# Kernel tuning notes

Measured on AMD Instinct MI355X. Metric: run time of the kernel, lower is better.

Reference implementation:

```python
import math
import jax, jax.numpy as jnp
import numpy as np

B, T, C, H, DQK, DV = 2, 2048, 1024, 16, 64, 64


def setup_inputs() -> dict:
    key = jax.random.key(0)
    ks = jax.random.split(key, 5)
    x = jax.random.normal(ks[0], (B, T, C), dtype=jnp.float32)
    # randw: randn(*d) / sqrt(d[-1])
    w_q = jax.random.normal(ks[1], (H, DQK, C), dtype=jnp.float32) / math.sqrt(C)
    w_k = jax.random.normal(ks[2], (H, DQK, C), dtype=jnp.float32) / math.sqrt(C)
    w_v = jax.random.normal(ks[3], (H, DV, C), dtype=jnp.float32) / math.sqrt(C)
    w_o = jax.random.normal(ks[4], (DV * H, C), dtype=jnp.float32) / math.sqrt(C)
    return {"x": x, "w_q": w_q, "w_k": w_k, "w_v": w_v, "w_o": w_o}


def reference(x, w_q, w_k, w_v, w_o):
    # Full-sequence causal forward (bs_q.first == 0, nb == T): caches are
    # fully written in one shot, so they reduce to the plain projections.
    n, t, c = x.shape
    q = jnp.einsum('ntc,hdc->nhtd', x, w_q)
    k = jnp.einsum('ntc,hdc->nhtd', x, w_k)
    v = jnp.einsum('ntc,hdc->nhtd', x, w_v)
    scale = 1.0 / math.sqrt(w_q.shape[1])
    a = jnp.einsum('nhtd,nhsd->nhts', q, k) * scale  # [n,h,t,s]
    causal = jnp.arange(t)[:, None] < jnp.arange(t)[None, :]  # True above diag
    a = jnp.where(causal[None, None, :, :], -jnp.inf, a)
    a = jax.nn.softmax(a, axis=3)
    y = jnp.einsum('nhts,nhsd->nthd', a, v).reshape(n, t, -1)  # [n,t,h*dv]
    return y @ w_o  # cache_y, [n,t,c]
```

## Files before the change

### kernel.cpp

```cpp
#include <hip/hip_runtime.h>


typedef short bf16x8 __attribute__((ext_vector_type(8)));
typedef float f32x4 __attribute__((ext_vector_type(4)));

#define MFMA_BF16 __builtin_amdgcn_mfma_f32_16x16x32_bf16

#define QSCALE 0.18033688011112042f

__device__ __forceinline__ unsigned short f2bf(float f) {
    union { float f; unsigned u; } un; un.f = f;
    unsigned r = un.u + 0x7fffu + ((un.u >> 16) & 1u);
    return (unsigned short)(r >> 16);
}
__device__ __forceinline__ unsigned short f2bf_trunc(float f) {
    union { float f; unsigned u; } un; un.f = f;
    return (unsigned short)(un.u >> 16);
}
__device__ __forceinline__ unsigned pk2(float a, float b) {
    return (unsigned)f2bf(a) | ((unsigned)f2bf(b) << 16);
}
__device__ __forceinline__ void gload16(const void* g, void* l) {
    __builtin_amdgcn_global_load_lds(
        (const __attribute__((address_space(1))) unsigned int*)g,
        (__attribute__((address_space(3))) unsigned int*)l, 16, 0, 0);
}

__global__ __launch_bounds__(256) void prep(
    const float* __restrict__ x, const float* __restrict__ wq,
    const float* __restrict__ wk, const float* __restrict__ wv,
    const float* __restrict__ wo,
    unsigned short* __restrict__ x16, unsigned short* __restrict__ wq16,
    unsigned short* __restrict__ wk16, unsigned short* __restrict__ wv16,
    unsigned short* __restrict__ wot)
{
    const int bid = blockIdx.x;
    if (bid < 3584) {
        const float* s; unsigned short* d; int off;
        if (bid < 2048)      { s = x;  d = x16;  off = bid * 2048; }
        else if (bid < 2560) { s = wq; d = wq16; off = (bid - 2048) * 2048; }
        else if (bid < 3072) { s = wk; d = wk16; off = (bid - 2560) * 2048; }
        else                 { s = wv; d = wv16; off = (bid - 3072) * 2048; }
        int i = off + threadIdx.x * 8;
        float4 f0 = *(const float4*)&s[i], f1 = *(const float4*)&s[i + 4];
        uint4 o;
        o.x = pk2(f0.x, f0.y); o.y = pk2(f0.z, f0.w);
        o.z = pk2(f1.x, f1.y); o.w = pk2(f1.z, f1.w);
        *(uint4*)&d[i] = o;
    } else {
        __shared__ unsigned short t[64 * 72];
        const int b2 = bid - 3584;
        const int k0 = (b2 & 15) << 6, n0 = (b2 >> 4) << 6;
        const int r = threadIdx.x >> 2, cg = (threadIdx.x & 3) << 4;
        const float* src = &wo[(k0 + r) * 1024 + n0 + cg];
        #pragma unroll
        for (int j = 0; j < 16; j += 4) {
            float4 f = *(const float4*)&src[j];
            t[(cg + j + 0) * 72 + r] = f2bf(f.x);
            t[(cg + j + 1) * 72 + r] = f2bf(f.y);
            t[(cg + j + 2) * 72 + r] = f2bf(f.z);
            t[(cg + j + 3) * 72 + r] = f2bf(f.w);
        }
        __syncthreads();
        unsigned short* dst = &wot[(n0 + r) * 1024 + k0 + cg];
        unsigned short* tr = &t[r * 72 + cg];
        unsigned v[16];
        #pragma unroll
        for (int j = 0; j < 16; ++j) v[j] = tr[j];
        uint4 o0, o1;
        o0.x = v[0] | (v[1] << 16);   o0.y = v[2] | (v[3] << 16);
        o0.z = v[4] | (v[5] << 16);   o0.w = v[6] | (v[7] << 16);
        o1.x = v[8] | (v[9] << 16);   o1.y = v[10] | (v[11] << 16);
        o1.z = v[12] | (v[13] << 16); o1.w = v[14] | (v[15] << 16);
        *(uint4*)&dst[0] = o0;
        *(uint4*)&dst[8] = o1;
    }
}

__device__ __forceinline__ void gemm_body(
    const unsigned short* __restrict__ A, const unsigned short* __restrict__ Bm,
    void* __restrict__ C, int m0, int n0, int mode, int ldc, float sc)
{
    __shared__ unsigned short sa[128 * 64];
    __shared__ unsigned short sb[128 * 64];
    const int tid = threadIdx.x, wave = tid >> 6, lane = tid & 63;
    const int l15 = lane & 15, l4 = lane >> 4;
    const int wm = (wave >> 1) << 6, wn = (wave & 1) << 6;
    const int lrow = lane >> 3, lcb = (lane & 7) << 3;

    f32x4 acc[4][4] = {};

    for (int k0 = 0; k0 < 1024; k0 += 64) {
        #pragma unroll
        for (int i = 0; i < 4; ++i) {
            int rbase = i * 32 + wave * 8;
            gload16(&A[(size_t)(m0 + rbase + lrow) * 1024 + k0 + lcb], &sa[rbase * 64]);
            gload16(&Bm[(size_t)(n0 + rbase + lrow) * 1024 + k0 + lcb], &sb[rbase * 64]);
        }
        __syncthreads();
        #pragma unroll
        for (int ks = 0; ks < 2; ++ks) {
            bf16x8 af[4], bf[4];
            #pragma unroll
            for (int i = 0; i < 4; ++i)
                af[i] = *(const bf16x8*)&sa[(wm + i * 16 + l15) * 64 + ks * 32 + l4 * 8];
            #pragma unroll
            for (int j = 0; j < 4; ++j)
                bf[j] = *(const bf16x8*)&sb[(wn + j * 16 + l15) * 64 + ks * 32 + l4 * 8];
            #pragma unroll
            for (int i = 0; i < 4; ++i)
                #pragma unroll
                for (int j = 0; j < 4; ++j)
                    acc[i][j] = MFMA_BF16(af[i], bf[j], acc[i][j], 0, 0, 0);
        }
        __syncthreads();
    }

    #pragma unroll
    for (int i = 0; i < 4; ++i)
        #pragma unroll
        for (int j = 0; j < 4; ++j)
            #pragma unroll
            for (int r = 0; r < 4; ++r) {
                int row = m0 + wm + i * 16 + l4 * 4 + r;
                int col = n0 + wn + j * 16 + l15;
                float val = acc[i][j][r];
                if (mode == 0) {
                    int nb = row >> 11, t = row & 2047;
                    int hh = col >> 6, dd = col & 63;
                    ((unsigned short*)C)[(((nb << 4) + hh) * 2048 + t) * 64 + dd] =
                        f2bf(val * sc);
                } else if (mode == 1) {
                    ((float*)C)[(size_t)row * ldc + col] = val;
                } else {
                    ((unsigned short*)C)[(size_t)row * ldc + col] = f2bf(val);
                }
            }
}

__global__ __launch_bounds__(256) void proj(
    const unsigned short* __restrict__ x16,
    const unsigned short* __restrict__ wq16,
    const unsigned short* __restrict__ wk16,
    const unsigned short* __restrict__ wv16,
    unsigned short* __restrict__ qbuf,
    unsigned short* __restrict__ kbuf,
    unsigned short* __restrict__ vtb)
{
    const int bid = blockIdx.x;
    if (bid < 512) {
        int m0 = (bid & 31) << 7;
        int n0g = (bid >> 5) << 7;
        if (n0g < 1024)
            gemm_body(x16, wq16, qbuf, m0, n0g, 0, 0, QSCALE);
        else
            gemm_body(x16, wk16, kbuf, m0, n0g - 1024, 0, 0, 1.0f);
    } else {
        int v = bid - 512;
        gemm_body(wv16, x16, vtb, (v & 7) << 7, (v >> 3) << 7, 2, 4096, 1.0f);
    }
}

__global__ __launch_bounds__(256) void outp(
    const unsigned short* __restrict__ ybuf,
    const unsigned short* __restrict__ wot,
    float* __restrict__ out)
{
    const int bid = blockIdx.x;
    gemm_body(ybuf, wot, out, (bid & 31) << 7, (bid >> 5) << 7, 1, 1024, 1.0f);
}

__global__ __launch_bounds__(256) void attn(
    const unsigned short* __restrict__ q,
    const unsigned short* __restrict__ k,
    const unsigned short* __restrict__ vt,
    unsigned short* __restrict__ y)
{
    constexpr int P = 72;
    __shared__ unsigned short sk[64 * P];
    __shared__ unsigned short sv[64 * P];
    __shared__ unsigned short sp[64 * P];
    const int tid = threadIdx.x, wave = tid >> 6, lane = tid & 63;
    const int l15 = lane & 15, l4 = lane >> 4;
    const int bid = blockIdx.x;
    const int qtt = (bid < 512) ? (31 - (bid >> 5)) : ((bid - 512) >> 5);
    const int bh = bid & 31;
    const int nb = bh >> 4, hh = bh & 15;
    const int q0 = qtt << 6;
    const size_t base = (size_t)bh << 17;

    bf16x8 qf[2];
    #pragma unroll
    for (int ks = 0; ks < 2; ++ks)
        qf[ks] = *(const bf16x8*)
            &q[base + (size_t)(q0 + wave * 16 + l15) * 64 + ks * 32 + l4 * 8];

    float l_part[4] = {0.f, 0.f, 0.f, 0.f};
    f32x4 acc_o[4] = {};

    const int nst = qtt + 1;
    for (int st = 0; st < nst; ++st) {
        const int s0 = st << 6;
        for (int vv = tid; vv < 512; vv += 256) {
            int row = vv >> 3, col = (vv & 7) << 3;
            *(uint4*)&sk[row * P + col] =
                *(const uint4*)&k[base + (size_t)((s0 + row) << 6) + col];
            *(uint4*)&sv[row * P + col] =
                *(const uint4*)&vt[(size_t)((hh << 6) + row) * 4096 + (nb << 11) + s0 + col];
        }
        __syncthreads();

        f32x4 s_acc[4] = {};
        #pragma unroll
        for (int ks = 0; ks < 2; ++ks)
            #pragma unroll
            for (int ns = 0; ns < 4; ++ns) {
                bf16x8 kf = *(const bf16x8*)&sk[(ns * 16 + l15) * P + ks * 32 + l4 * 8];
                s_acc[ns] = MFMA_BF16(qf[ks], kf, s_acc[ns], 0, 0, 0);
            }

        if (st == qtt) {
            #pragma unroll
            for (int ns = 0; ns < 4; ++ns) {
                const int cl = ns * 16 + l15;
                #pragma unroll
                for (int r = 0; r < 4; ++r) {
                    const int rl = wave * 16 + l4 * 4 + r;
                    if (cl > rl) s_acc[ns][r] = -1e30f;
                }
            }
        }

        #pragma unroll
        for (int r = 0; r < 4; ++r) {
            float p0 = exp2f(s_acc[0][r]);
            float p1 = exp2f(s_acc[1][r]);
            float p2 = exp2f(s_acc[2][r]);
            float p3 = exp2f(s_acc[3][r]);
            const int rowl = (wave * 16 + l4 * 4 + r) * P;
            sp[rowl +  0 + l15] = f2bf_trunc(p0);
            sp[rowl + 16 + l15] = f2bf_trunc(p1);
            sp[rowl + 32 + l15] = f2bf_trunc(p2);
            sp[rowl + 48 + l15] = f2bf_trunc(p3);
            l_part[r] += (p0 + p1) + (p2 + p3);
        }

        #pragma unroll
        for (int ks = 0; ks < 2; ++ks) {
            bf16x8 pf = *(const bf16x8*)&sp[(wave * 16 + l15) * P + ks * 32 + l4 * 8];
            #pragma unroll
            for (int ds = 0; ds < 4; ++ds) {
                bf16x8 vf = *(const bf16x8*)&sv[(ds * 16 + l15) * P + ks * 32 + l4 * 8];
                acc_o[ds] = MFMA_BF16(pf, vf, acc_o[ds], 0, 0, 0);
            }
        }
        __syncthreads();
    }

    float rl[4];
    #pragma unroll
    for (int r = 0; r < 4; ++r) {
        float s = l_part[r];
        #pragma unroll
        for (int off = 1; off < 16; off <<= 1) s += __shfl_xor(s, off);
        rl[r] = __builtin_amdgcn_rcpf(s);
    }
    #pragma unroll
    for (int ds = 0; ds < 4; ++ds)
        #pragma unroll
        for (int r = 0; r < 4; ++r) {
            const int rg = q0 + wave * 16 + l4 * 4 + r;
            y[((size_t)((nb << 11) + rg) << 10) + (hh << 6) + ds * 16 + l15] =
                f2bf(acc_o[ds][r] * rl[r]);
        }
}

extern "C" void kernel_launch(void* const* d_in, const int* in_sizes, int n_in,
                              void* d_out, int out_size, void* d_ws, size_t ws_size,
                              hipStream_t stream) {
    const float* x  = (const float*)d_in[0];
    const float* wq = (const float*)d_in[1];
    const float* wk = (const float*)d_in[2];
    const float* wv = (const float*)d_in[3];
    const float* wo = (const float*)d_in[4];
    float* out = (float*)d_out;

    const size_t M1 = 1u << 20;
    unsigned short* x16  = (unsigned short*)d_ws;
    unsigned short* wq16 = x16 + 4 * M1;
    unsigned short* wk16 = wq16 + M1;
    unsigned short* wv16 = wk16 + M1;
    unsigned short* wot  = wv16 + M1;
    unsigned short* qbuf = wot + M1;
    unsigned short* kbuf = qbuf + 4 * M1;
    unsigned short* vtb  = kbuf + 4 * M1;
    unsigned short* ybuf = vtb + 4 * M1;

    dim3 blk(256);
    prep<<<3840, blk, 0, stream>>>(x, wq, wk, wv, wo, x16, wq16, wk16, wv16, wot);
    proj<<<768, blk, 0, stream>>>(x16, wq16, wk16, wv16, qbuf, kbuf, vtb);
    attn<<<1024, blk, 0, stream>>>(qbuf, kbuf, vtb, ybuf);
    outp<<<256, blk, 0, stream>>>(ybuf, wot, out);
}
```

Measured before the change: 210.4 us.

## Use 64x128 tiles for output projection and swizzle P tile in attention

The output projection is replaced with a dedicated GEMM using 64x128 tiles, doubling the grid from 256 to 512 blocks so more compute units are busy on the 4096x1024x1024 product. Operand tiles are loaded with direct global-to-LDS loads, and there is no software pipelining. Separately, the attention kernel XOR-swizzles column indices when writing and reading the probability tile in shared memory, to reduce LDS bank conflicts. The swizzle has to match between the scalar writes and the vector reads, otherwise the P·V results are wrong.

```diff
diff --git a/kernel.cpp b/kernel.cpp
--- a/kernel.cpp
+++ b/kernel.cpp
@@ -166,8 +166,48 @@
     const unsigned short* __restrict__ wot,
     float* __restrict__ out)
 {
+    __shared__ unsigned short sa[64 * 64];
+    __shared__ unsigned short sb[128 * 64];
+    const int tid = threadIdx.x, wave = tid >> 6, lane = tid & 63;
+    const int l15 = lane & 15, l4 = lane >> 4;
     const int bid = blockIdx.x;
-    gemm_body(ybuf, wot, out, (bid & 31) << 7, (bid >> 5) << 7, 1, 1024, 1.0f);
+    const int m0 = (bid & 63) << 6, n0 = (bid >> 6) << 7;
+    const int lrow = lane >> 3, lcb = (lane & 7) << 3;
+
+    f32x4 acc[8] = {};
+
+    for (int k0 = 0; k0 < 1024; k0 += 64) {
+        #pragma unroll
+        for (int i = 0; i < 2; ++i) {
+            int rbase = i * 32 + wave * 8;
+            gload16(&ybuf[(size_t)(m0 + rbase + lrow) * 1024 + k0 + lcb], &sa[rbase * 64]);
+        }
+        #pragma unroll
+        for (int i = 0; i < 4; ++i) {
+            int rbase = i * 32 + wave * 8;
+            gload16(&wot[(size_t)(n0 + rbase + lrow) * 1024 + k0 + lcb], &sb[rbase * 64]);
+        }
+        __syncthreads();
+        #pragma unroll
+        for (int ks = 0; ks < 2; ++ks) {
+            bf16x8 af = *(const bf16x8*)&sa[(wave * 16 + l15) * 64 + ks * 32 + l4 * 8];
+            #pragma unroll
+            for (int j = 0; j < 8; ++j) {
+                bf16x8 bf = *(const bf16x8*)&sb[(j * 16 + l15) * 64 + ks * 32 + l4 * 8];
+                acc[j] = MFMA_BF16(af, bf, acc[j], 0, 0, 0);
+            }
+        }
+        __syncthreads();
+    }
+
+    #pragma unroll
+    for (int j = 0; j < 8; ++j)
+        #pragma unroll
+        for (int r = 0; r < 4; ++r) {
+            int row = m0 + wave * 16 + l4 * 4 + r;
+            int col = n0 + j * 16 + l15;
+            out[(size_t)row * 1024 + col] = acc[j][r];
+        }
 }
 
 __global__ __launch_bounds__(256) void attn(
@@ -198,6 +238,9 @@
     float l_part[4] = {0.f, 0.f, 0.f, 0.f};
     f32x4 acc_o[4] = {};
 
+    const int swW = (l4 & 2) << 3;
+    const int swR = (l15 & 8) << 1;
+
     const int nst = qtt + 1;
     for (int st = 0; st < nst; ++st) {
         const int s0 = st << 6;
@@ -238,16 +281,17 @@
             float p2 = exp2f(s_acc[2][r]);
             float p3 = exp2f(s_acc[3][r]);
             const int rowl = (wave * 16 + l4 * 4 + r) * P;
-            sp[rowl +  0 + l15] = f2bf_trunc(p0);
-            sp[rowl + 16 + l15] = f2bf_trunc(p1);
-            sp[rowl + 32 + l15] = f2bf_trunc(p2);
-            sp[rowl + 48 + l15] = f2bf_trunc(p3);
+            sp[rowl + (( 0 + l15) ^ swW)] = f2bf_trunc(p0);
+            sp[rowl + ((16 + l15) ^ swW)] = f2bf_trunc(p1);
+            sp[rowl + ((32 + l15) ^ swW)] = f2bf_trunc(p2);
+            sp[rowl + ((48 + l15) ^ swW)] = f2bf_trunc(p3);
             l_part[r] += (p0 + p1) + (p2 + p3);
         }
 
         #pragma unroll
         for (int ks = 0; ks < 2; ++ks) {
-            bf16x8 pf = *(const bf16x8*)&sp[(wave * 16 + l15) * P + ks * 32 + l4 * 8];
+            bf16x8 pf = *(const bf16x8*)
+                &sp[(wave * 16 + l15) * P + ((ks * 32 + l4 * 8) ^ swR)];
             #pragma unroll
             for (int ds = 0; ds < 4; ++ds) {
                 bf16x8 vf = *(const bf16x8*)&sv[(ds * 16 + l15) * P + ks * 32 + l4 * 8];
@@ -300,5 +344,5 @@
     prep<<<3840, blk, 0, stream>>>(x, wq, wk, wv, wo, x16, wq16, wk16, wv16, wot);
     proj<<<768, blk, 0, stream>>>(x16, wq16, wk16, wv16, qbuf, kbuf, vtb);
     attn<<<1024, blk, 0, stream>>>(qbuf, kbuf, vtb, ybuf);
-    outp<<<256, blk, 0, stream>>>(ybuf, wot, out);
-}
+    outp<<<512, blk, 0, stream>>>(ybuf, wot, out);
+}
```

New measurement: 215.7 us. 1.03x slower.
